# Kernel optimization log

Hardware: AMD Instinct MI355X
Metric: run time of the kernel (lower is better)

## Reference

```python
import jax, jax.numpy as jnp
import numpy as np

N_NODE = 100000
N_EDGE = 800000
IN_DIM = 128
OUT_DIM = 128
ATTN_DIM = 64
N_REL = 200
N_ENT = 40000
BATCH = 64
N_RELA_ROWS = 2 * N_REL + 1  # 401


def setup_inputs() -> dict:
    key = jax.random.key(0)
    ks = jax.random.split(key, 16)
    # edges: [E, 6] -> col0: r_idx (batch idx), col2: rel, col4: sub, col5: obj
    r_idx = jax.random.randint(ks[0], (N_EDGE,), 0, BATCH)
    rel = jax.random.randint(ks[1], (N_EDGE,), 0, N_RELA_ROWS)
    sub = jax.random.randint(ks[2], (N_EDGE,), 0, N_NODE)
    obj = jax.random.randint(ks[3], (N_EDGE,), 0, N_NODE)
    zeros_col = jnp.zeros((N_EDGE,), dtype=jnp.int32)
    edges = jnp.stack([r_idx, zeros_col, rel, zeros_col, sub, obj], axis=1)

    hidden = jax.random.normal(ks[4], (N_NODE, IN_DIM), dtype=jnp.float32)
    q_sub = jax.random.randint(ks[5], (BATCH,), 0, N_ENT)
    q_rel = jax.random.randint(ks[6], (BATCH,), 0, N_RELA_ROWS)
    nodes = jnp.stack([
        jax.random.randint(ks[7], (N_NODE,), 0, BATCH),
        jax.random.randint(ks[8], (N_NODE,), 0, N_ENT)], axis=1)
    old_nodes_new_idx = jax.random.randint(ks[9], (50000,), 0, N_NODE)

    s = 0.05
    rela_embed = jax.random.normal(ks[10], (N_RELA_ROWS, IN_DIM), dtype=jnp.float32) * s
    Ws = jax.random.normal(ks[11], (IN_DIM, ATTN_DIM), dtype=jnp.float32) * s
    Wr = jax.random.normal(ks[12], (IN_DIM, ATTN_DIM), dtype=jnp.float32) * s
    Wqr = jax.random.normal(ks[13], (IN_DIM, ATTN_DIM), dtype=jnp.float32) * s
    bqr = jnp.zeros((ATTN_DIM,), dtype=jnp.float32)
    wa = jax.random.normal(ks[14], (ATTN_DIM, 1), dtype=jnp.float32) * s
    ba = jnp.zeros((1,), dtype=jnp.float32)
    W_h = jax.random.normal(ks[15], (IN_DIM, OUT_DIM), dtype=jnp.float32) * s

    return {"q_sub": q_sub, "q_rel": q_rel, "hidden": hidden, "edges": edges,
            "nodes": nodes, "old_nodes_new_idx": old_nodes_new_idx, "batchsize": BATCH,
            "rela_embed": rela_embed, "Ws": Ws, "Wr": Wr, "Wqr": Wqr, "bqr": bqr,
            "wa": wa, "ba": ba, "W_h": W_h}


def reference(q_sub, q_rel, hidden, edges, nodes, old_nodes_new_idx, batchsize,
              rela_embed, Ws, Wr, Wqr, bqr, wa, ba, W_h):
    sub = edges[:, 4]
    rel = edges[:, 2]
    obj = edges[:, 5]
    r_idx = edges[:, 0]
    n_node = nodes.shape[0]

    hs = hidden[sub]                    # [E, in_dim]  gather
    hr = rela_embed[rel]                # [E, in_dim]
    h_qr = rela_embed[q_rel][r_idx]     # [E, in_dim]

    # MESS_FUNC == 'TransE'
    message = hs + hr

    # attention MLP: sigmoid(w_alpha(relu(Ws hs + Wr hr + Wqr h_qr + bqr)))
    attn = jax.nn.relu(hs @ Ws + hr @ Wr + h_qr @ Wqr + bqr)  # [E, attn_dim]
    alpha = jax.nn.sigmoid(attn @ wa + ba)                     # [E, 1]
    message = alpha * message

    # AGG_FUNC == 'max': scatter-max into node buckets, empty buckets -> 0
    agg = jax.ops.segment_max(message, obj, num_segments=n_node)
    agg = jnp.where(jnp.isneginf(agg), 0.0, agg)

    # COMB_FUNC == 'discard', act is identity
    hidden_new = agg @ W_h              # [n_node, out_dim]
    return hidden_new
```

## Files before the change

### kernel.cpp

```cpp
#include <hip/hip_runtime.h>
#include <hip/hip_fp16.h>

#define N_NODE 100000
#define N_EDGE 800000
#define IN_DIM 128
#define OUT_DIM 128
#define ATTN 64
#define N_RELA 401
#define BATCH 64
#define CAP 32
#define CSTR 16

#define SW_BLOCKS 6250
#define RELQ_BLOCKS 117
#define CNT_BLOCKS 3125
#define WH_BLOCKS 16

typedef _Float16 half8 __attribute__((ext_vector_type(8)));
typedef _Float16 h2 __attribute__((ext_vector_type(2)));
typedef float f32x4 __attribute__((ext_vector_type(4)));

#if __has_builtin(__builtin_elementwise_max)
#define H2MAX(a, b) __builtin_elementwise_max((a), (b))
#else
#define H2MAX(a, b) (((a) > (b)) ? (a) : (b))
#endif

__device__ __forceinline__ unsigned short f2h(float f) {
    return __half_as_ushort(__float2half_rn(f));
}
__device__ __forceinline__ unsigned pack_h2(float lo, float hi) {
    return (unsigned)f2h(lo) | ((unsigned)f2h(hi) << 16);
}

__global__ __launch_bounds__(256) void k_prep(
    const float* __restrict__ hidden, const float* __restrict__ Ws,
    unsigned short* __restrict__ sW_h, unsigned* __restrict__ hid_h,
    const float* __restrict__ rela, const float* __restrict__ Wr,
    const float* __restrict__ Wqr, const float* __restrict__ bqr,
    const int* __restrict__ q_rel, unsigned short* __restrict__ rW_h,
    unsigned short* __restrict__ qW_h, unsigned* __restrict__ rel_h,
    const int* __restrict__ edges, int* __restrict__ cnt,
    unsigned* __restrict__ rec, const float* __restrict__ W_h,
    unsigned* __restrict__ W_hT_h) {
    const int b = blockIdx.x;
    if (b < SW_BLOCKS) {
        const int wvu = __builtin_amdgcn_readfirstlane((int)(threadIdx.x >> 6));
        const int t = threadIdx.x & 63;
        const long base = ((long)b * 4 + wvu) * 4;
        const float* hbase = hidden + base * IN_DIM;
#pragma unroll
        for (int j = 0; j < 4; ++j) {
            const float2 pv = *(const float2*)(hbase + j * IN_DIM + 2 * t);
            hid_h[(base + j) * 64 + t] = pack_h2(pv.x, pv.y);
        }
        float acc[4] = {0.f, 0.f, 0.f, 0.f};
        for (int kq = 0; kq < IN_DIM / 4; ++kq) {
            const float w0 = Ws[(4 * kq + 0) * ATTN + t];
            const float w1 = Ws[(4 * kq + 1) * ATTN + t];
            const float w2 = Ws[(4 * kq + 2) * ATTN + t];
            const float w3 = Ws[(4 * kq + 3) * ATTN + t];
#pragma unroll
            for (int j = 0; j < 4; ++j) {
                const float4 av = *(const float4*)(hbase + j * IN_DIM + 4 * kq);
                acc[j] = fmaf(av.x, w0, acc[j]);
                acc[j] = fmaf(av.y, w1, acc[j]);
                acc[j] = fmaf(av.z, w2, acc[j]);
                acc[j] = fmaf(av.w, w3, acc[j]);
            }
        }
#pragma unroll
        for (int j = 0; j < 4; ++j) sW_h[(base + j) * ATTN + t] = f2h(acc[j]);
    } else if (b < SW_BLOCKS + RELQ_BLOCKS) {
        const int wv = threadIdx.x >> 6;
        const int t = threadIdx.x & 63;
        const int row = (b - SW_BLOCKS) * 4 + wv;
        if (row >= N_RELA + BATCH) return;
        if (row < N_RELA) {
            const float* hrow = rela + (long)row * IN_DIM;
            float acc = 0.f;
            for (int k = 0; k < IN_DIM; ++k) acc = fmaf(hrow[k], Wr[k * ATTN + t], acc);
            rW_h[row * ATTN + t] = f2h(acc);
            rel_h[row * 64 + t] = pack_h2(hrow[2 * t], hrow[2 * t + 1]);
        } else {
            const int q = row - N_RELA;
            const float* hrow = rela + (long)q_rel[q] * IN_DIM;
            float acc = bqr[t];
            for (int k = 0; k < IN_DIM; ++k) acc = fmaf(hrow[k], Wqr[k * ATTN + t], acc);
            qW_h[q * ATTN + t] = f2h(acc);
        }
    } else if (b < SW_BLOCKS + RELQ_BLOCKS + CNT_BLOCKS) {
        const int e = (b - SW_BLOCKS - RELQ_BLOCKS) * 256 + threadIdx.x;
        if (e >= N_EDGE) return;
        const int* ed = edges + (long)e * 6;
        const int2 p0 = *(const int2*)(ed);
        const int2 p1 = *(const int2*)(ed + 2);
        const int2 p2 = *(const int2*)(ed + 4);
        const unsigned pk =
            ((unsigned)p2.x << 15) | ((unsigned)p1.x << 6) | (unsigned)p0.x;
        const int slot = atomicAdd(&cnt[(unsigned)p2.y * CSTR], 1);
        if (slot < CAP) rec[(unsigned)p2.y * CAP + slot] = pk;
    } else {
        const int t0 = (b - SW_BLOCKS - RELQ_BLOCKS - CNT_BLOCKS) * 256 + threadIdx.x;
#pragma unroll
        for (int i = 0; i < 2; ++i) {
            const int d = t0 * 2 + i;
            const int c = d >> 6;
            const int dd = d & 63;
            const float lo = W_h[(2 * dd) * OUT_DIM + c];
            const float hi = W_h[(2 * dd + 1) * OUT_DIM + c];
            W_hT_h[d] = pack_h2(lo, hi);
        }
    }
}

__global__ __launch_bounds__(512) void k_fused(const unsigned* __restrict__ rec,
                                               const int* __restrict__ cnt,
                                               const unsigned* __restrict__ hid_h,
                                               const unsigned* __restrict__ rel_h,
                                               const unsigned short* __restrict__ sW_h,
                                               const unsigned short* __restrict__ rW_h,
                                               const unsigned short* __restrict__ qW_h,
                                               const float* __restrict__ wa,
                                               const float* __restrict__ ba,
                                               unsigned* __restrict__ agg_h) {
    const int lane = threadIdx.x & 63;
    const int wv = threadIdx.x >> 6;
    const int l8 = lane & 7;
    const int grp = lane >> 3;
    const unsigned node = (unsigned)blockIdx.x * 8 + wv;
    const int deg = min(cnt[node * CSTR], CAP);
    const float4 wv0 = ((const float4*)wa)[l8 * 2];
    const float4 wv1 = ((const float4*)wa)[l8 * 2 + 1];
    const h2 wah0 = {(_Float16)wv0.x, (_Float16)wv0.y};
    const h2 wah1 = {(_Float16)wv0.z, (_Float16)wv0.w};
    const h2 wah2 = {(_Float16)wv1.x, (_Float16)wv1.y};
    const h2 wah3 = {(_Float16)wv1.z, (_Float16)wv1.w};
    const h2 zh = {(_Float16)0.f, (_Float16)0.f};
    const float bav = ba[0];
    const uint4* sW4 = (const uint4*)sW_h;
    const uint4* rW4 = (const uint4*)rW_h;
    const uint4* qW4 = (const uint4*)qW_h;
    h2 m = {(_Float16)(-65504.f), (_Float16)(-65504.f)};

    if (deg > 0) {
        const unsigned myrec = rec[node * CAP + (unsigned)min(lane, deg - 1)];
        for (int i = 0; i < deg; i += 8) {
            const int gi = min(i + grp, deg - 1);
            const unsigned rg = __shfl(myrec, gi);
            const uint4 s4 = sW4[(rg >> 15) * 8u + (unsigned)l8];
            const uint4 r4 = rW4[((rg >> 6) & 511u) * 8u + (unsigned)l8];
            const uint4 q4 = qW4[(rg & 63u) * 8u + (unsigned)l8];
            unsigned hs[8], hr[8];
#pragma unroll
            for (int k = 0; k < 8; ++k) {
                const unsigned rrk = __shfl(myrec, min(i + k, deg - 1));
                hs[k] = hid_h[(rrk >> 15) * 64u + (unsigned)lane];
                hr[k] = rel_h[((rrk >> 6) & 511u) * 64u + (unsigned)lane];
            }
            h2 t0 = __builtin_bit_cast(h2, s4.x) + __builtin_bit_cast(h2, r4.x) +
                    __builtin_bit_cast(h2, q4.x);
            h2 t1 = __builtin_bit_cast(h2, s4.y) + __builtin_bit_cast(h2, r4.y) +
                    __builtin_bit_cast(h2, q4.y);
            h2 t2 = __builtin_bit_cast(h2, s4.z) + __builtin_bit_cast(h2, r4.z) +
                    __builtin_bit_cast(h2, q4.z);
            h2 t3 = __builtin_bit_cast(h2, s4.w) + __builtin_bit_cast(h2, r4.w) +
                    __builtin_bit_cast(h2, q4.w);
            t0 = H2MAX(t0, zh);
            t1 = H2MAX(t1, zh);
            t2 = H2MAX(t2, zh);
            t3 = H2MAX(t3, zh);
#if __has_builtin(__builtin_amdgcn_fdot2)
            float p = __builtin_amdgcn_fdot2(t0, wah0, 0.f, false);
            p = __builtin_amdgcn_fdot2(t1, wah1, p, false);
            p = __builtin_amdgcn_fdot2(t2, wah2, p, false);
            p = __builtin_amdgcn_fdot2(t3, wah3, p, false);
#else
            float p = (float)t0.x * wv0.x;
            p = fmaf((float)t0.y, wv0.y, p);
            p = fmaf((float)t1.x, wv0.z, p);
            p = fmaf((float)t1.y, wv0.w, p);
            p = fmaf((float)t2.x, wv1.x, p);
            p = fmaf((float)t2.y, wv1.y, p);
            p = fmaf((float)t3.x, wv1.z, p);
            p = fmaf((float)t3.y, wv1.w, p);
#endif
            p += __shfl_xor(p, 1);
            p += __shfl_xor(p, 2);
            p += __shfl_xor(p, 4);
            const float al_own = 1.f / (1.f + __expf(-(p + bav)));
            const int nb = deg - i;
#pragma unroll
            for (int k = 0; k < 8; ++k) {
                if (k == 0 || nb > k) {
                    const _Float16 alh = (_Float16)__shfl(al_own, k * 8);
                    const h2 av = {alh, alh};
                    const h2 msg = __builtin_bit_cast(h2, hs[k]) +
                                   __builtin_bit_cast(h2, hr[k]);
                    m = H2MAX(m, av * msg);
                }
            }
        }
    } else {
        m = zh;
    }
    agg_h[node * 64u + (unsigned)lane] = __builtin_bit_cast(unsigned, m);
}

__global__ __launch_bounds__(128) void k_out(const unsigned* __restrict__ agg_h,
                                             const unsigned* __restrict__ W_hT_h,
                                             float* __restrict__ out) {
    const int wv = threadIdx.x >> 6;
    const int lane = threadIdx.x & 63;
    const int l15 = lane & 15;
    const int lh = lane >> 4;
    const int rb = (blockIdx.x * 2 + wv) * 16;
    const unsigned* AU = agg_h + (unsigned)(rb + l15) * 64u + (unsigned)(lh * 4);
    half8 af[4];
#pragma unroll
    for (int kk = 0; kk < 4; ++kk) af[kk] = *(const half8*)(AU + kk * 16);
#pragma unroll
    for (int n = 0; n < 8; ++n) {
        const unsigned* BU = W_hT_h + (unsigned)(n * 16 + l15) * 64u + (unsigned)(lh * 4);
        f32x4 acc = {0.f, 0.f, 0.f, 0.f};
#pragma unroll
        for (int kk = 0; kk < 4; ++kk)
            acc = __builtin_amdgcn_mfma_f32_16x16x32_f16(
                af[kk], *(const half8*)(BU + kk * 16), acc, 0, 0, 0);
        float* op = out + (long)(rb + lh * 4) * OUT_DIM + n * 16 + l15;
        op[0] = acc[0];
        op[OUT_DIM] = acc[1];
        op[2 * OUT_DIM] = acc[2];
        op[3 * OUT_DIM] = acc[3];
    }
}

extern "C" void kernel_launch(void* const* d_in, const int* in_sizes, int n_in,
                              void* d_out, int out_size, void* d_ws, size_t ws_size,
                              hipStream_t stream) {
    const int* q_rel = (const int*)d_in[1];
    const float* hidden = (const float*)d_in[2];
    const int* edges = (const int*)d_in[3];
    const float* rela = (const float*)d_in[7];
    const float* Ws = (const float*)d_in[8];
    const float* Wr = (const float*)d_in[9];
    const float* Wqr = (const float*)d_in[10];
    const float* bqr = (const float*)d_in[11];
    const float* wa = (const float*)d_in[12];
    const float* ba = (const float*)d_in[13];
    const float* W_h = (const float*)d_in[14];
    float* out = (float*)d_out;

    char* ws = (char*)d_ws;
    unsigned short* sW_h = (unsigned short*)(ws);
    unsigned* hid_h = (unsigned*)(ws + 12800000);
    unsigned* rel_h = (unsigned*)(ws + 38400000);
    unsigned short* rW_h = (unsigned short*)(ws + 38502656);
    unsigned short* qW_h = (unsigned short*)(ws + 38553984);
    int* cnt = (int*)(ws + 38562176);
    unsigned* rec = (unsigned*)(ws + 44962176);
    unsigned* agg_h = (unsigned*)(ws + 57762176);
    unsigned* W_hT_h = (unsigned*)(ws + 83362176);

    hipMemsetAsync(cnt, 0, (size_t)N_NODE * CSTR * sizeof(int), stream);
    hipLaunchKernelGGL(k_prep,
                       dim3(SW_BLOCKS + RELQ_BLOCKS + CNT_BLOCKS + WH_BLOCKS),
                       dim3(256), 0, stream, hidden, Ws, sW_h, hid_h, rela, Wr,
                       Wqr, bqr, q_rel, rW_h, qW_h, rel_h, edges, cnt, rec,
                       W_h, W_hT_h);
    hipLaunchKernelGGL(k_fused, dim3(N_NODE / 8), dim3(512), 0, stream,
                       rec, cnt, hid_h, rel_h, sW_h, rW_h, qW_h, wa, ba,
                       agg_h);
    hipLaunchKernelGGL(k_out, dim3(3125), dim3(128), 0, stream,
                       agg_h, W_hT_h, out);
}
```

Measured before the change: 286.8 us.

## Fuse output projection into aggregation kernel via LDS-staged MFMA

The separate k_out GEMM kernel is removed. Each 4-wave block now stages its four aggregated node rows in LDS and multiplies them by W_h with MFMA, each wave covering two output column tiles. This drops the agg_h round-trip through global memory and one kernel launch. In exchange, block size falls to 256, and the 16-row MFMA tiles carry only 4 valid rows, so most of the matrix work is wasted and W_h is re-read once per block.

Result: slower. 325.2 us (+13.4%).

```diff
diff --git a/kernel.cpp b/kernel.cpp
--- a/kernel.cpp
+++ b/kernel.cpp
@@ -114,7 +114,7 @@
     }
 }
 
-__global__ __launch_bounds__(512) void k_fused(const unsigned* __restrict__ rec,
+__global__ __launch_bounds__(256) void k_fused(const unsigned* __restrict__ rec,
                                                const int* __restrict__ cnt,
                                                const unsigned* __restrict__ hid_h,
                                                const unsigned* __restrict__ rel_h,
@@ -123,12 +123,14 @@
                                                const unsigned short* __restrict__ qW_h,
                                                const float* __restrict__ wa,
                                                const float* __restrict__ ba,
-                                               unsigned* __restrict__ agg_h) {
+                                               const unsigned* __restrict__ W_hT_h,
+                                               float* __restrict__ out) {
+    __shared__ __align__(16) unsigned a_lds[4][68];
     const int lane = threadIdx.x & 63;
     const int wv = threadIdx.x >> 6;
     const int l8 = lane & 7;
     const int grp = lane >> 3;
-    const unsigned node = (unsigned)blockIdx.x * 8 + wv;
+    const unsigned node = (unsigned)blockIdx.x * 4 + wv;
     const int deg = min(cnt[node * CSTR], CAP);
     const float4 wv0 = ((const float4*)wa)[l8 * 2];
     const float4 wv1 = ((const float4*)wa)[l8 * 2 + 1];
@@ -204,34 +206,35 @@
     } else {
         m = zh;
     }
-    agg_h[node * 64u + (unsigned)lane] = __builtin_bit_cast(unsigned, m);
-}
-
-__global__ __launch_bounds__(128) void k_out(const unsigned* __restrict__ agg_h,
-                                             const unsigned* __restrict__ W_hT_h,
-                                             float* __restrict__ out) {
-    const int wv = threadIdx.x >> 6;
-    const int lane = threadIdx.x & 63;
-    const int l15 = lane & 15;
-    const int lh = lane >> 4;
-    const int rb = (blockIdx.x * 2 + wv) * 16;
-    const unsigned* AU = agg_h + (unsigned)(rb + l15) * 64u + (unsigned)(lh * 4);
-    half8 af[4];
-#pragma unroll
-    for (int kk = 0; kk < 4; ++kk) af[kk] = *(const half8*)(AU + kk * 16);
-#pragma unroll
-    for (int n = 0; n < 8; ++n) {
-        const unsigned* BU = W_hT_h + (unsigned)(n * 16 + l15) * 64u + (unsigned)(lh * 4);
-        f32x4 acc = {0.f, 0.f, 0.f, 0.f};
+    a_lds[wv][lane] = __builtin_bit_cast(unsigned, m);
+    __syncthreads();
+    {
+        const int l15 = lane & 15;
+        const int lh = lane >> 4;
+        const int ar = l15 & 3;
+        half8 af[4];
 #pragma unroll
         for (int kk = 0; kk < 4; ++kk)
-            acc = __builtin_amdgcn_mfma_f32_16x16x32_f16(
-                af[kk], *(const half8*)(BU + kk * 16), acc, 0, 0, 0);
-        float* op = out + (long)(rb + lh * 4) * OUT_DIM + n * 16 + l15;
-        op[0] = acc[0];
-        op[OUT_DIM] = acc[1];
-        op[2 * OUT_DIM] = acc[2];
-        op[3 * OUT_DIM] = acc[3];
+            af[kk] = *(const half8*)&a_lds[ar][lh * 4 + kk * 16];
+        const long nb4 = (long)blockIdx.x * 4;
+#pragma unroll
+        for (int nn = 0; nn < 2; ++nn) {
+            const int nt = wv * 2 + nn;
+            const unsigned* BU =
+                W_hT_h + (unsigned)(nt * 16 + l15) * 64u + (unsigned)(lh * 4);
+            f32x4 acc = {0.f, 0.f, 0.f, 0.f};
+#pragma unroll
+            for (int kk = 0; kk < 4; ++kk)
+                acc = __builtin_amdgcn_mfma_f32_16x16x32_f16(
+                    af[kk], *(const half8*)(BU + kk * 16), acc, 0, 0, 0);
+            if (lh == 0) {
+                float* op = out + nb4 * OUT_DIM + nt * 16 + l15;
+                op[0] = acc[0];
+                op[OUT_DIM] = acc[1];
+                op[2 * OUT_DIM] = acc[2];
+                op[3 * OUT_DIM] = acc[3];
+            }
+        }
     }
 }
 
@@ -259,8 +262,7 @@
     unsigned short* qW_h = (unsigned short*)(ws + 38553984);
     int* cnt = (int*)(ws + 38562176);
     unsigned* rec = (unsigned*)(ws + 44962176);
-    unsigned* agg_h = (unsigned*)(ws + 57762176);
-    unsigned* W_hT_h = (unsigned*)(ws + 83362176);
+    unsigned* W_hT_h = (unsigned*)(ws + 57762176);
 
     hipMemsetAsync(cnt, 0, (size_t)N_NODE * CSTR * sizeof(int), stream);
     hipLaunchKernelGGL(k_prep,
@@ -268,9 +270,7 @@
                        dim3(256), 0, stream, hidden, Ws, sW_h, hid_h, rela, Wr,
                        Wqr, bqr, q_rel, rW_h, qW_h, rel_h, edges, cnt, rec,
                        W_h, W_hT_h);
-    hipLaunchKernelGGL(k_fused, dim3(N_NODE / 8), dim3(512), 0, stream,
+    hipLaunchKernelGGL(k_fused, dim3(N_NODE / 4), dim3(256), 0, stream,
                        rec, cnt, hid_h, rel_h, sW_h, rW_h, qW_h, wa, ba,
-                       agg_h);
-    hipLaunchKernelGGL(k_out, dim3(3125), dim3(128), 0, stream,
-                       agg_h, W_hT_h, out);
-}
+                       W_hT_h, out);
+}
```
